# Kernel tuning notes

Hardware: AMD Instinct MI355X
Metric: run time of the kernel (lower is better)

The kernel has to match this reference:

```python
import jax, jax.numpy as jnp
import numpy as np

B, S, E, H = 8, 2048, 1024, 64

def setup_inputs() -> dict:
    key = jax.random.key(0)
    ks = jax.random.split(key, 10)
    inp = {
        'input_Q': jax.random.normal(ks[0], (B, S, E), dtype=jnp.float32),
        'input_K': jax.random.normal(ks[1], (B, S, E), dtype=jnp.float32),
        'input_V': jax.random.normal(ks[2], (B, S, E), dtype=jnp.float32),
        'mask': jax.random.randint(ks[3], (B, S, S), 0, 2) > 0,
        # Linear params: torch Linear(E, H) -> weight [H, E], use as x @ W^T + b; store transposed [E, H]
        'Wq': jax.random.normal(ks[4], (E, H), dtype=jnp.float32) / np.sqrt(E),
        'bq': jnp.zeros((H,), dtype=jnp.float32),
        'Wk': jax.random.normal(ks[5], (E, H), dtype=jnp.float32) / np.sqrt(E),
        'bk': jnp.zeros((H,), dtype=jnp.float32),
        'Wv': jax.random.normal(ks[6], (E, H), dtype=jnp.float32) / np.sqrt(E),
        'bv': jnp.zeros((H,), dtype=jnp.float32),
    }
    return inp

def reference(input_Q, input_K, input_V, mask, Wq, bq, Wk, bk, Wv, bv):
    Q = jnp.einsum('bse,eh->bsh', input_Q, Wq) + bq  # [B,S,H]
    K = jnp.einsum('bse,eh->bsh', input_K, Wk) + bk
    V = jnp.einsum('bse,eh->bsh', input_V, Wv) + bv
    scores = jnp.einsum('bqh,bkh->bqk', Q, K) / np.sqrt(H).astype(np.float32)  # [B,S,S]
    # faithful to masked_fill_(mask, 1e-10) BEFORE softmax
    scores = jnp.where(mask, jnp.float32(1e-10), scores)
    attn = jax.nn.softmax(scores, axis=-1)
    # dropout is identity in eval/reference mode
    return jnp.einsum('bqk,bkh->bqh', attn, V)
```

## Files before the change

kernel.cpp:

```cpp
#include <hip/hip_runtime.h>
#include <hip/hip_bf16.h>
#include <stdint.h>

constexpr int Bc = 8, Sc = 2048, Ec = 1024, Hc = 64;

typedef __bf16 bf16x8 __attribute__((ext_vector_type(8)));
typedef float f32x4 __attribute__((ext_vector_type(4)));
typedef unsigned short ushort8 __attribute__((ext_vector_type(8)));
typedef unsigned short ushort4v __attribute__((ext_vector_type(4)));
typedef uint32_t uint32x4 __attribute__((ext_vector_type(4)));

static __device__ __forceinline__ unsigned short f2bf(float f) {
  uint32_t u = __builtin_bit_cast(uint32_t, f);
  u = u + 0x7fffu + ((u >> 16) & 1u);
  return (unsigned short)(u >> 16);
}
static __device__ __forceinline__ bf16x8 ldb8(const unsigned short* p) {
  return __builtin_bit_cast(bf16x8, *(const ushort8*)p);
}
static __device__ __forceinline__ uint32_t pk2bf(float a, float b) {
  return (uint32_t)f2bf(a) | ((uint32_t)f2bf(b) << 16);
}

__global__ __launch_bounds__(256) void wt_kernel(
    const float* __restrict__ Wq, const float* __restrict__ Wk,
    const float* __restrict__ Wv, unsigned short* __restrict__ Wt) {
  int idx = blockIdx.x * 256 + threadIdx.x;
  int m = idx >> 16;
  int r = idx & 65535;
  int h = r >> 10;
  int e = r & 1023;
  const float* W = (m == 0) ? Wq : (m == 1) ? Wk : Wv;
  float scale = (m == 0) ? 0.125f : 1.0f;
  Wt[idx] = f2bf(W[e * Hc + h] * scale);
}

__global__ __launch_bounds__(256, 8) void proj_kernel(
    const float* __restrict__ Xq, const float* __restrict__ Xk,
    const float* __restrict__ Xv, const float* __restrict__ bq,
    const float* __restrict__ bk, const float* __restrict__ bv,
    const unsigned short* __restrict__ Wt,
    unsigned short* __restrict__ Qb, unsigned short* __restrict__ Kb,
    unsigned short* __restrict__ Vt) {
  const int mat = blockIdx.y;
  const float* X = (mat == 0) ? Xq : (mat == 1) ? Xk : Xv;
  const float* bias = (mat == 0) ? bq : (mat == 1) ? bk : bv;
  const float bscale = (mat == 0) ? 0.125f : 1.0f;
  const unsigned short* W = Wt + mat * (Hc * Ec);

  const int tid = threadIdx.x;
  const int wave = tid >> 6, lane = tid & 63;
  const int rl = lane & 15, kg = lane >> 4;
  const int row0 = blockIdx.x * 16;
  const int kw = wave * 256;

  __shared__ float slab[4][16][64];

  const float* xp = X + (size_t)(row0 + rl) * Ec + kw + kg * 8;
  const unsigned short* wp0 = W + (size_t)(0 * 16 + rl) * Ec + kw + kg * 8;
  const unsigned short* wp1 = W + (size_t)(1 * 16 + rl) * Ec + kw + kg * 8;
  const unsigned short* wp2 = W + (size_t)(2 * 16 + rl) * Ec + kw + kg * 8;
  const unsigned short* wp3 = W + (size_t)(3 * 16 + rl) * Ec + kw + kg * 8;

  f32x4 acc[4];
#pragma unroll
  for (int nt = 0; nt < 4; nt++) acc[nt] = (f32x4){0.f, 0.f, 0.f, 0.f};

#pragma unroll
  for (int c = 0; c < 8; c++) {
    float4 x0 = *(const float4*)(xp + c * 32);
    float4 x1 = *(const float4*)(xp + c * 32 + 4);
    ushort8 w0 = *(const ushort8*)(wp0 + c * 32);
    ushort8 w1 = *(const ushort8*)(wp1 + c * 32);
    ushort8 w2 = *(const ushort8*)(wp2 + c * 32);
    ushort8 w3 = *(const ushort8*)(wp3 + c * 32);
    uint32x4 u = (uint32x4){pk2bf(x0.x, x0.y), pk2bf(x0.z, x0.w),
                            pk2bf(x1.x, x1.y), pk2bf(x1.z, x1.w)};
    bf16x8 aX = __builtin_bit_cast(bf16x8, u);
    acc[0] = __builtin_amdgcn_mfma_f32_16x16x32_bf16(
        aX, __builtin_bit_cast(bf16x8, w0), acc[0], 0, 0, 0);
    acc[1] = __builtin_amdgcn_mfma_f32_16x16x32_bf16(
        aX, __builtin_bit_cast(bf16x8, w1), acc[1], 0, 0, 0);
    acc[2] = __builtin_amdgcn_mfma_f32_16x16x32_bf16(
        aX, __builtin_bit_cast(bf16x8, w2), acc[2], 0, 0, 0);
    acc[3] = __builtin_amdgcn_mfma_f32_16x16x32_bf16(
        aX, __builtin_bit_cast(bf16x8, w3), acc[3], 0, 0, 0);
  }

#pragma unroll
  for (int nt = 0; nt < 4; nt++)
#pragma unroll
    for (int r = 0; r < 4; r++)
      slab[wave][kg * 4 + r][nt * 16 + rl] = acc[nt][r];
  __syncthreads();

  if (mat < 2) {
    unsigned short* out = (mat == 0) ? Qb : Kb;
    int row = wave * 4 + (lane >> 4);
    int col0 = (lane & 15) * 4;
    f32x4 s0 = *(const f32x4*)&slab[0][row][col0];
    f32x4 s1 = *(const f32x4*)&slab[1][row][col0];
    f32x4 s2 = *(const f32x4*)&slab[2][row][col0];
    f32x4 s3 = *(const f32x4*)&slab[3][row][col0];
    float4 bv4 = *(const float4*)(bias + col0);
    f32x4 v = s0 + s1 + s2 + s3;
    v[0] += bv4.x * bscale; v[1] += bv4.y * bscale;
    v[2] += bv4.z * bscale; v[3] += bv4.w * bscale;
    ushort4v o;
#pragma unroll
    for (int i = 0; i < 4; i++) o[i] = f2bf(v[i]);
    *(ushort4v*)(out + (size_t)(row0 + row) * Hc + col0) = o;
  } else {
    int h = lane;
    int bb = row0 >> 11;
    int sbase = (row0 & 2047) + wave * 4;
    float bh = bias[h];
    ushort4v o;
#pragma unroll
    for (int r = 0; r < 4; r++) {
      float v = slab[0][wave * 4 + r][h] + slab[1][wave * 4 + r][h] +
                slab[2][wave * 4 + r][h] + slab[3][wave * 4 + r][h] + bh;
      o[r] = f2bf(v);
    }
    *(ushort4v*)(Vt + ((size_t)bb * Hc + h) * Sc + sbase) = o;
  }
}

__global__ __launch_bounds__(256, 4) void attn_kernel(
    const unsigned short* __restrict__ Qb, const unsigned short* __restrict__ Kb,
    const unsigned short* __restrict__ Vt, const int* __restrict__ mask,
    float* __restrict__ out) {
  const int id = blockIdx.x;
  const int b = id & 7;
  const int q0 = (id >> 3) * 16;
  const int tid = threadIdx.x;
  const int wave = tid >> 6, lane = tid & 63;

  __shared__ unsigned short Ps[4][16][72];
  __shared__ float sm[4][16], sl[4][16];
  __shared__ float Os[4][16][64];

  const unsigned short* qptr =
      Qb + ((size_t)b * Sc + q0 + (lane & 15)) * Hc + (lane >> 4) * 8;
  bf16x8 aQ0 = ldb8(qptr);
  bf16x8 aQ1 = ldb8(qptr + 32);

  float m_r[4], l_r[4];
  f32x4 Oacc[4];
#pragma unroll
  for (int r = 0; r < 4; r++) { m_r[r] = -INFINITY; l_r[r] = 0.f; }
#pragma unroll
  for (int ht = 0; ht < 4; ht++) Oacc[ht] = (f32x4){0.f, 0.f, 0.f, 0.f};

  const int* mrow[4];
#pragma unroll
  for (int r = 0; r < 4; r++)
    mrow[r] = mask + ((size_t)b * Sc + q0 + (lane >> 4) * 4 + r) * Sc + (lane & 15);

  const unsigned short* kbase =
      Kb + ((size_t)b * Sc) * Hc + (size_t)(lane & 15) * Hc + (lane >> 4) * 8;
  const unsigned short* vbase[4];
#pragma unroll
  for (int ht = 0; ht < 4; ht++)
    vbase[ht] = Vt + ((size_t)b * Hc + ht * 16 + (lane & 15)) * Sc + (lane >> 4) * 8;

  const int kw = wave * 512;
  int mva[4][4], mvb[4][4];

  auto issue_mask = [&](int koff, int (&mv)[4][4]) {
#pragma unroll
    for (int nt = 0; nt < 4; nt++)
#pragma unroll
      for (int r = 0; r < 4; r++) mv[nt][r] = mrow[r][koff + nt * 16];
  };
  auto compress = [&](const int (&mv)[4][4]) -> uint32_t {
    uint32_t bits = 0;
#pragma unroll
    for (int nt = 0; nt < 4; nt++)
#pragma unroll
      for (int r = 0; r < 4; r++)
        bits |= (mv[nt][r] ? 1u : 0u) << (nt * 4 + r);
    return bits;
  };

  auto process = [&](int koff, uint32_t bits) {
    float sv[4][4];
#pragma unroll
    for (int nt = 0; nt < 4; nt++) {
      const unsigned short* kp = kbase + (size_t)(koff + nt * 16) * Hc;
      bf16x8 bK0 = ldb8(kp);
      bf16x8 bK1 = ldb8(kp + 32);
      f32x4 s = (f32x4){0.f, 0.f, 0.f, 0.f};
      s = __builtin_amdgcn_mfma_f32_16x16x32_bf16(aQ0, bK0, s, 0, 0, 0);
      s = __builtin_amdgcn_mfma_f32_16x16x32_bf16(aQ1, bK1, s, 0, 0, 0);
#pragma unroll
      for (int r = 0; r < 4; r++)
        sv[nt][r] = ((bits >> (nt * 4 + r)) & 1u) ? 1e-10f : s[r];
    }

    float rmax[4];
#pragma unroll
    for (int r = 0; r < 4; r++) {
      rmax[r] = fmaxf(fmaxf(sv[0][r], sv[1][r]), fmaxf(sv[2][r], sv[3][r]));
#pragma unroll
      for (int off = 1; off < 16; off <<= 1)
        rmax[r] = fmaxf(rmax[r], __shfl_xor(rmax[r], off, 64));
    }

    float alpha[4], p[4][4], psum[4];
#pragma unroll
    for (int r = 0; r < 4; r++) {
      float mnew = fmaxf(m_r[r], rmax[r]);
      alpha[r] = __expf(m_r[r] - mnew);
      m_r[r] = mnew;
      psum[r] = 0.f;
    }
#pragma unroll
    for (int nt = 0; nt < 4; nt++)
#pragma unroll
      for (int r = 0; r < 4; r++) {
        p[nt][r] = __expf(sv[nt][r] - m_r[r]);
        psum[r] += p[nt][r];
      }
#pragma unroll
    for (int r = 0; r < 4; r++) {
#pragma unroll
      for (int off = 1; off < 16; off <<= 1)
        psum[r] += __shfl_xor(psum[r], off, 64);
      l_r[r] = l_r[r] * alpha[r] + psum[r];
    }
#pragma unroll
    for (int ht = 0; ht < 4; ht++)
#pragma unroll
      for (int r = 0; r < 4; r++) Oacc[ht][r] *= alpha[r];

#pragma unroll
    for (int nt = 0; nt < 4; nt++)
#pragma unroll
      for (int r = 0; r < 4; r++)
        Ps[wave][(lane >> 4) * 4 + r][nt * 16 + (lane & 15)] = f2bf(p[nt][r]);

#pragma unroll
    for (int ks = 0; ks < 2; ks++) {
      bf16x8 aP = ldb8(&Ps[wave][lane & 15][ks * 32 + (lane >> 4) * 8]);
#pragma unroll
      for (int ht = 0; ht < 4; ht++) {
        bf16x8 bV = ldb8(vbase[ht] + koff + ks * 32);
        Oacc[ht] = __builtin_amdgcn_mfma_f32_16x16x32_bf16(aP, bV, Oacc[ht], 0, 0, 0);
      }
    }
  };

  issue_mask(kw, mva);
  for (int c2 = 0; c2 < 8; c2 += 2) {
    issue_mask(kw + (c2 + 1) * 64, mvb);
    process(kw + c2 * 64, compress(mva));
    if (c2 + 2 < 8) issue_mask(kw + (c2 + 2) * 64, mva);
    process(kw + (c2 + 1) * 64, compress(mvb));
  }

  if ((lane & 15) == 0) {
#pragma unroll
    for (int r = 0; r < 4; r++) {
      sm[wave][(lane >> 4) * 4 + r] = m_r[r];
      sl[wave][(lane >> 4) * 4 + r] = l_r[r];
    }
  }
  __syncthreads();

  float coef[4];
#pragma unroll
  for (int r = 0; r < 4; r++) {
    int row = (lane >> 4) * 4 + r;
    float M = fmaxf(fmaxf(sm[0][row], sm[1][row]), fmaxf(sm[2][row], sm[3][row]));
    coef[r] = __expf(m_r[r] - M);
  }
#pragma unroll
  for (int ht = 0; ht < 4; ht++)
#pragma unroll
    for (int r = 0; r < 4; r++)
      Os[wave][(lane >> 4) * 4 + r][ht * 16 + (lane & 15)] = Oacc[ht][r] * coef[r];
  __syncthreads();

  {
#pragma unroll
    for (int i = 0; i < 4; i++) {
      int row = wave * 4 + i;
      float M = fmaxf(fmaxf(sm[0][row], sm[1][row]), fmaxf(sm[2][row], sm[3][row]));
      float L = sl[0][row] * __expf(sm[0][row] - M) +
                sl[1][row] * __expf(sm[1][row] - M) +
                sl[2][row] * __expf(sm[2][row] - M) +
                sl[3][row] * __expf(sm[3][row] - M);
      float acc = Os[0][row][lane] + Os[1][row][lane] +
                  Os[2][row][lane] + Os[3][row][lane];
      out[((size_t)b * Sc + q0 + row) * Hc + lane] = acc / L;
    }
  }
}

extern "C" void kernel_launch(void* const* d_in, const int* in_sizes, int n_in,
                              void* d_out, int out_size, void* d_ws, size_t ws_size,
                              hipStream_t stream) {
  const float* Xq = (const float*)d_in[0];
  const float* Xk = (const float*)d_in[1];
  const float* Xv = (const float*)d_in[2];
  const int* mask = (const int*)d_in[3];
  const float* Wq = (const float*)d_in[4];
  const float* bq = (const float*)d_in[5];
  const float* Wk = (const float*)d_in[6];
  const float* bk = (const float*)d_in[7];
  const float* Wv = (const float*)d_in[8];
  const float* bv = (const float*)d_in[9];

  unsigned short* Qb = (unsigned short*)d_ws;
  unsigned short* Kb = Qb + (size_t)Bc * Sc * Hc;
  unsigned short* Vt = Kb + (size_t)Bc * Sc * Hc;
  unsigned short* Wt = Vt + (size_t)Bc * Sc * Hc;

  wt_kernel<<<dim3(3 * Hc * Ec / 256), 256, 0, stream>>>(Wq, Wk, Wv, Wt);
  proj_kernel<<<dim3(Bc * Sc / 16, 3), 256, 0, stream>>>(Xq, Xk, Xv, bq, bk, bv,
                                                         Wt, Qb, Kb, Vt);
  attn_kernel<<<dim3(Bc * Sc / 16), 256, 0, stream>>>(Qb, Kb, Vt, mask,
                                                      (float*)d_out);
}
```

Measured before the change: 410.1 us.

## Precompute packed mask bits and stage projection inputs in swizzled LDS

```diff
diff --git a/kernel.cpp b/kernel.cpp
--- a/kernel.cpp
+++ b/kernel.cpp
@@ -35,7 +35,23 @@
   Wt[idx] = f2bf(W[e * Hc + h] * scale);
 }
 
-__global__ __launch_bounds__(256, 8) void proj_kernel(
+__global__ __launch_bounds__(256) void mask_kernel(
+    const int* __restrict__ mask, uint32_t* __restrict__ Mb) {
+  int w = blockIdx.x * 256 + threadIdx.x;
+  const int* src = mask + (size_t)w * 32;
+  uint32_t bits = 0;
+#pragma unroll
+  for (int i = 0; i < 8; i++) {
+    int4 v = *(const int4*)(src + i * 4);
+    bits |= (v.x ? 1u : 0u) << (i * 4 + 0);
+    bits |= (v.y ? 1u : 0u) << (i * 4 + 1);
+    bits |= (v.z ? 1u : 0u) << (i * 4 + 2);
+    bits |= (v.w ? 1u : 0u) << (i * 4 + 3);
+  }
+  Mb[w] = bits;
+}
+
+__global__ __launch_bounds__(256, 5) void proj_kernel(
     const float* __restrict__ Xq, const float* __restrict__ Xk,
     const float* __restrict__ Xv, const float* __restrict__ bq,
     const float* __restrict__ bk, const float* __restrict__ bv,
@@ -54,9 +70,23 @@
   const int row0 = blockIdx.x * 16;
   const int kw = wave * 256;
 
-  __shared__ float slab[4][16][64];
-
-  const float* xp = X + (size_t)(row0 + rl) * Ec + kw + kg * 8;
+  __shared__ __align__(16) char smem[32768];
+
+  const float* xsrc = X + (size_t)row0 * Ec;
+#pragma unroll
+  for (int i = 0; i < 16; i++) {
+    int idx = i * 256 + tid;
+    float4 v = *(const float4*)(xsrc + (size_t)idx * 4);
+    int f = idx * 4;
+    int row = f >> 10, col = f & 1023;
+    uint32_t byte = (uint32_t)(row * 2048 + col * 2) ^ (uint32_t)((row & 7) << 4);
+    uint2 pk;
+    pk.x = pk2bf(v.x, v.y);
+    pk.y = pk2bf(v.z, v.w);
+    *(uint2*)(smem + byte) = pk;
+  }
+  __syncthreads();
+
   const unsigned short* wp0 = W + (size_t)(0 * 16 + rl) * Ec + kw + kg * 8;
   const unsigned short* wp1 = W + (size_t)(1 * 16 + rl) * Ec + kw + kg * 8;
   const unsigned short* wp2 = W + (size_t)(2 * 16 + rl) * Ec + kw + kg * 8;
@@ -68,15 +98,13 @@
 
 #pragma unroll
   for (int c = 0; c < 8; c++) {
-    float4 x0 = *(const float4*)(xp + c * 32);
-    float4 x1 = *(const float4*)(xp + c * 32 + 4);
+    int col = kw + kg * 8 + c * 32;
+    uint32_t byte = (uint32_t)(rl * 2048 + col * 2) ^ (uint32_t)((rl & 7) << 4);
+    bf16x8 aX = *(const bf16x8*)(smem + byte);
     ushort8 w0 = *(const ushort8*)(wp0 + c * 32);
     ushort8 w1 = *(const ushort8*)(wp1 + c * 32);
     ushort8 w2 = *(const ushort8*)(wp2 + c * 32);
     ushort8 w3 = *(const ushort8*)(wp3 + c * 32);
-    uint32x4 u = (uint32x4){pk2bf(x0.x, x0.y), pk2bf(x0.z, x0.w),
-                            pk2bf(x1.x, x1.y), pk2bf(x1.z, x1.w)};
-    bf16x8 aX = __builtin_bit_cast(bf16x8, u);
     acc[0] = __builtin_amdgcn_mfma_f32_16x16x32_bf16(
         aX, __builtin_bit_cast(bf16x8, w0), acc[0], 0, 0, 0);
     acc[1] = __builtin_amdgcn_mfma_f32_16x16x32_bf16(
@@ -87,6 +115,8 @@
         aX, __builtin_bit_cast(bf16x8, w3), acc[3], 0, 0, 0);
   }
 
+  __syncthreads();
+  float (*slab)[16][64] = (float (*)[16][64])smem;
 #pragma unroll
   for (int nt = 0; nt < 4; nt++)
 #pragma unroll
@@ -128,20 +158,21 @@
 
 __global__ __launch_bounds__(256, 4) void attn_kernel(
     const unsigned short* __restrict__ Qb, const unsigned short* __restrict__ Kb,
-    const unsigned short* __restrict__ Vt, const int* __restrict__ mask,
+    const unsigned short* __restrict__ Vt, const uint32_t* __restrict__ Mb,
     float* __restrict__ out) {
   const int id = blockIdx.x;
   const int b = id & 7;
   const int q0 = (id >> 3) * 16;
   const int tid = threadIdx.x;
   const int wave = tid >> 6, lane = tid & 63;
+  const int rl = lane & 15;
 
   __shared__ unsigned short Ps[4][16][72];
   __shared__ float sm[4][16], sl[4][16];
   __shared__ float Os[4][16][64];
 
   const unsigned short* qptr =
-      Qb + ((size_t)b * Sc + q0 + (lane & 15)) * Hc + (lane >> 4) * 8;
+      Qb + ((size_t)b * Sc + q0 + rl) * Hc + (lane >> 4) * 8;
   bf16x8 aQ0 = ldb8(qptr);
   bf16x8 aQ1 = ldb8(qptr + 32);
 
@@ -152,34 +183,35 @@
 #pragma unroll
   for (int ht = 0; ht < 4; ht++) Oacc[ht] = (f32x4){0.f, 0.f, 0.f, 0.f};
 
-  const int* mrow[4];
+  const uint32_t* mbase[4];
 #pragma unroll
   for (int r = 0; r < 4; r++)
-    mrow[r] = mask + ((size_t)b * Sc + q0 + (lane >> 4) * 4 + r) * Sc + (lane & 15);
+    mbase[r] = Mb + ((size_t)b * Sc + q0 + (lane >> 4) * 4 + r) * 64;
 
   const unsigned short* kbase =
-      Kb + ((size_t)b * Sc) * Hc + (size_t)(lane & 15) * Hc + (lane >> 4) * 8;
+      Kb + ((size_t)b * Sc) * Hc + (size_t)rl * Hc + (lane >> 4) * 8;
   const unsigned short* vbase[4];
 #pragma unroll
   for (int ht = 0; ht < 4; ht++)
-    vbase[ht] = Vt + ((size_t)b * Hc + ht * 16 + (lane & 15)) * Sc + (lane >> 4) * 8;
+    vbase[ht] = Vt + ((size_t)b * Hc + ht * 16 + rl) * Sc + (lane >> 4) * 8;
 
   const int kw = wave * 512;
-  int mva[4][4], mvb[4][4];
-
-  auto issue_mask = [&](int koff, int (&mv)[4][4]) {
-#pragma unroll
-    for (int nt = 0; nt < 4; nt++)
-#pragma unroll
-      for (int r = 0; r < 4; r++) mv[nt][r] = mrow[r][koff + nt * 16];
+  uint2 mva[4], mvb[4];
+
+  auto issue_mask = [&](int koff, uint2 (&mv)[4]) {
+#pragma unroll
+    for (int r = 0; r < 4; r++)
+      mv[r] = *(const uint2*)(mbase[r] + (koff >> 5));
   };
-  auto compress = [&](const int (&mv)[4][4]) -> uint32_t {
+  auto compress = [&](const uint2 (&mv)[4]) -> uint32_t {
     uint32_t bits = 0;
 #pragma unroll
-    for (int nt = 0; nt < 4; nt++)
-#pragma unroll
-      for (int r = 0; r < 4; r++)
-        bits |= (mv[nt][r] ? 1u : 0u) << (nt * 4 + r);
+    for (int r = 0; r < 4; r++) {
+      bits |= ((mv[r].x >> rl) & 1u) << (0 + r);
+      bits |= ((mv[r].x >> (16 + rl)) & 1u) << (4 + r);
+      bits |= ((mv[r].y >> rl) & 1u) << (8 + r);
+      bits |= ((mv[r].y >> (16 + rl)) & 1u) << (12 + r);
+    }
     return bits;
   };
 
@@ -238,11 +270,11 @@
     for (int nt = 0; nt < 4; nt++)
 #pragma unroll
       for (int r = 0; r < 4; r++)
-        Ps[wave][(lane >> 4) * 4 + r][nt * 16 + (lane & 15)] = f2bf(p[nt][r]);
+        Ps[wave][(lane >> 4) * 4 + r][nt * 16 + rl] = f2bf(p[nt][r]);
 
 #pragma unroll
     for (int ks = 0; ks < 2; ks++) {
-      bf16x8 aP = ldb8(&Ps[wave][lane & 15][ks * 32 + (lane >> 4) * 8]);
+      bf16x8 aP = ldb8(&Ps[wave][rl][ks * 32 + (lane >> 4) * 8]);
 #pragma unroll
       for (int ht = 0; ht < 4; ht++) {
         bf16x8 bV = ldb8(vbase[ht] + koff + ks * 32);
@@ -259,7 +291,7 @@
     process(kw + (c2 + 1) * 64, compress(mvb));
   }
 
-  if ((lane & 15) == 0) {
+  if (rl == 0) {
 #pragma unroll
     for (int r = 0; r < 4; r++) {
       sm[wave][(lane >> 4) * 4 + r] = m_r[r];
@@ -279,7 +311,7 @@
   for (int ht = 0; ht < 4; ht++)
 #pragma unroll
     for (int r = 0; r < 4; r++)
-      Os[wave][(lane >> 4) * 4 + r][ht * 16 + (lane & 15)] = Oacc[ht][r] * coef[r];
+      Os[wave][(lane >> 4) * 4 + r][ht * 16 + rl] = Oacc[ht][r] * coef[r];
   __syncthreads();
 
   {
@@ -316,10 +348,12 @@
   unsigned short* Kb = Qb + (size_t)Bc * Sc * Hc;
   unsigned short* Vt = Kb + (size_t)Bc * Sc * Hc;
   unsigned short* Wt = Vt + (size_t)Bc * Sc * Hc;
+  uint32_t* Mb = (uint32_t*)(Wt + (size_t)3 * Hc * Ec);
 
   wt_kernel<<<dim3(3 * Hc * Ec / 256), 256, 0, stream>>>(Wq, Wk, Wv, Wt);
+  mask_kernel<<<dim3(Bc * Sc * (Sc / 32) / 256), 256, 0, stream>>>(mask, Mb);
   proj_kernel<<<dim3(Bc * Sc / 16, 3), 256, 0, stream>>>(Xq, Xk, Xv, bq, bk, bv,
                                                          Wt, Qb, Kb, Vt);
-  attn_kernel<<<dim3(Bc * Sc / 16), 256, 0, stream>>>(Qb, Kb, Vt, mask,
+  attn_kernel<<<dim3(Bc * Sc / 16), 256, 0, stream>>>(Qb, Kb, Vt, Mb,
                                                       (float*)d_out);
 }
```

New measurement: 424.3 us. +3.5%, slower.
